# Performance work log

Measured on AMD Instinct MI355X. Metric: run time of the kernel, lower is better.

The kernel has to match this reference:

```python
import jax, jax.numpy as jnp
import numpy as np

BATCH, SEQ, D_MODEL, STATE_DIM = 2, 4096, 1024, 16
LN_EPS = 1e-5
IMP_TEMP = 0.5


def setup_inputs() -> dict:
    key = jax.random.key(0)
    ks = jax.random.split(key, 7)
    std = 0.02
    x = jax.random.normal(ks[0], (BATCH, SEQ, D_MODEL), jnp.float32)
    A_log = jax.random.normal(ks[1], (D_MODEL, STATE_DIM), jnp.float32) * 0.1
    # Linear weights stored as [in, out] so y = x @ W (same math as torch x @ W.T)
    W_delta = jax.random.normal(ks[2], (D_MODEL, D_MODEL), jnp.float32) * std
    W_B = jax.random.normal(ks[3], (D_MODEL, STATE_DIM), jnp.float32) * std
    W_C = jax.random.normal(ks[4], (D_MODEL, STATE_DIM), jnp.float32) * std
    W_ctx = jax.random.normal(ks[5], (D_MODEL, D_MODEL), jnp.float32) * std
    W_imp = jax.random.normal(ks[6], (D_MODEL, D_MODEL), jnp.float32) * std
    ln_gamma = jnp.ones((D_MODEL,), jnp.float32)
    ln_beta = jnp.zeros((D_MODEL,), jnp.float32)
    context_scale = jnp.asarray(0.1, jnp.float32)
    return dict(x=x, A_log=A_log, W_delta=W_delta, W_B=W_B, W_C=W_C,
                ln_gamma=ln_gamma, ln_beta=ln_beta, W_ctx=W_ctx,
                context_scale=context_scale, W_imp=W_imp)


def _selective_scan(x, delta, A, B_sel, C_sel):
    # x, delta: [B,S,D]; A: [D,N]; B_sel, C_sel: [B,S,N]
    Bsz, S, D = x.shape
    N = A.shape[1]
    h0 = jnp.zeros((Bsz, D, N), x.dtype)

    def step(h, inp):
        d_t, x_t, b_t, c_t = inp  # [B,D],[B,D],[B,N],[B,N]
        decay = jnp.exp(d_t[:, :, None] * A)             # [B,D,N]
        h = h * decay + (d_t * x_t)[:, :, None] * b_t[:, None, :]
        y = jnp.einsum('bdn,bn->bd', h, c_t)
        return h, y

    xs = (delta.transpose(1, 0, 2), x.transpose(1, 0, 2),
          B_sel.transpose(1, 0, 2), C_sel.transpose(1, 0, 2))
    _, ys = jax.lax.scan(step, h0, xs)                    # ys: [S,B,D]
    return ys.transpose(1, 0, 2)


def _layernorm(x, gamma, beta):
    mu = jnp.mean(x, axis=-1, keepdims=True)
    var = jnp.mean((x - mu) ** 2, axis=-1, keepdims=True)
    return (x - mu) * jax.lax.rsqrt(var + LN_EPS) * gamma + beta


def reference(x, A_log, W_delta, W_B, W_C, ln_gamma, ln_beta, W_ctx, context_scale, W_imp):
    delta = jax.nn.softplus(x @ W_delta)          # [B,S,D]
    B_sel = x @ W_B                               # [B,S,N]
    C_sel = x @ W_C                               # [B,S,N]
    A = -jnp.exp(A_log)                           # [D,N]
    ssm_out = _selective_scan(x, delta, A, B_sel, C_sel)
    ssm_out = _layernorm(ssm_out, ln_gamma, ln_beta)
    h_final = ssm_out[:, -1, :]                   # [B,D]
    h_proj = h_final @ W_imp                      # [B,D]
    raw_importance = jnp.einsum('bsd,bd->bs', x, h_proj)
    importance = jax.nn.softmax(raw_importance / IMP_TEMP, axis=-1)
    context = (ssm_out @ W_ctx) * context_scale
    return importance, context, raw_importance
```

## Files before the change

kernel.cpp:

```cpp
#include <hip/hip_runtime.h>
#include <hip/hip_bf16.h>
#include <stdint.h>

#define DEV static __device__ __forceinline__

typedef unsigned short u16;
typedef __bf16 bf16x8 __attribute__((ext_vector_type(8)));
typedef float f32x4 __attribute__((ext_vector_type(4)));
typedef u16 u16x8 __attribute__((ext_vector_type(8)));
typedef u16 u16x4 __attribute__((ext_vector_type(4)));

#define IMP_OFF 0
#define CTX_OFF 8192
#define RAW_OFF 8396800

DEV float b2f(u16 u) {
    union { unsigned int i; float f; } v; v.i = ((unsigned int)u) << 16; return v.f;
}
DEV u16 f2b(float f) {
    union { float f; unsigned int i; } v; v.f = f;
    unsigned int r = v.i + 0x7fffu + ((v.i >> 16) & 1u);
    return (u16)(r >> 16);
}
DEV u16 f2h(float f) {
    union { _Float16 h; u16 u; } v; v.h = (_Float16)f; return v.u;
}
DEV float h2f(u16 u) {
    union { u16 u; _Float16 h; } v; v.u = u; return (float)v.h;
}
DEV float softplus_f(float z) {
    float a = fabsf(z);
    return fmaxf(z, 0.f) + __logf(1.f + __expf(-a));
}
DEV float ldin(const void* p, size_t i, int f32) {
    return f32 ? ((const float*)p)[i] : b2f(((const u16*)p)[i]);
}
DEV void stout(void* base, size_t i, float v, int f32) {
    if (f32) ((float*)base)[i] = v;
    else     ((u16*)base)[i] = f2b(v);
}

typedef __attribute__((address_space(1))) void as1_void;
typedef __attribute__((address_space(3))) void as3_void;
DEV void gld_lds16(const void* g, void* l) {
    __builtin_amdgcn_global_load_lds((as1_void*)g, (as3_void*)l, 16, 0, 0);
}

__global__ void init_k(const void* gamma, const void* scale, int* flg, float* hproj)
{
    int i = blockIdx.x * 256 + threadIdx.x;
    if (i < 2048) hproj[i] = 0.f;
    if (i == 0) {
        unsigned int g = *(const unsigned int*)gamma;
        flg[0] = (g == 0x3F800000u) ? 1 : 0;
        unsigned int s = *(const unsigned int*)scale;
        flg[1] = (s == 0x3DCCCCCDu) ? 1 : 0;
    }
}

__global__ __launch_bounds__(256) void transpose_k(
    const void* __restrict__ s0, const void* __restrict__ s1,
    u16* __restrict__ d0, u16* __restrict__ d1, const int* __restrict__ flg)
{
    __shared__ u16 tile[32][33];
    int f32 = flg[0];
    int blk = blockIdx.x;
    const void* src = (blk < 1024) ? s0 : s1;
    u16* dst = (blk < 1024) ? d0 : d1;
    int t = blk & 1023;
    int tr = t >> 5, tc = t & 31;
    int lx = threadIdx.x & 31, ly = threadIdx.x >> 5;
    int r0 = tr * 32, c0 = tc * 32;
#pragma unroll
    for (int i = 0; i < 32; i += 8)
        tile[ly + i][lx] = f2b(ldin(src, (size_t)(r0 + ly + i) * 1024 + c0 + lx, f32));
    __syncthreads();
#pragma unroll
    for (int i = 0; i < 32; i += 8)
        dst[(size_t)(c0 + ly + i) * 1024 + r0 + lx] = tile[lx][ly + i];
}

__global__ __launch_bounds__(256) void prep_small_k(
    const void* __restrict__ W_B, const void* __restrict__ W_C,
    u16* __restrict__ WdT, const int* __restrict__ flg)
{
    int f32 = flg[0];
    int r = blockIdx.x;
    u16* dst = WdT + (size_t)(1024 + r) * 1024;
#pragma unroll
    for (int i = 0; i < 4; i++) {
        int d = threadIdx.x + i * 256;
        u16 v;
        if (r < 16)       v = f2b(ldin(W_B, (size_t)d * 16 + r, f32));
        else if (r < 32)  v = f2b(ldin(W_C, (size_t)d * 16 + (r - 16), f32));
        else              v = 0;
        dst[d] = v;
    }
}

#define GK 1024
__global__ __launch_bounds__(256) void gemm_bt(
    const void* __restrict__ Av, const u16* __restrict__ BT,
    u16* __restrict__ deltaOut, float* __restrict__ Bsel, float* __restrict__ Csel,
    void* __restrict__ outB, const void* __restrict__ scale_p,
    const int* __restrict__ flg, int nbn, int mode)
{
    __shared__ u16 lA[128 * 32];
    __shared__ u16 lB[128 * 32];
    int af32 = (mode == 0) ? flg[0] : 0;
    int blk = blockIdx.x;
    int xcd = blk & 7;
    int local = blk >> 3;
    int bm = xcd * 8 + local / nbn;
    int bn = local % nbn;
    int tid = threadIdx.x;
    int wave = tid >> 6, lane = tid & 63;
    int wm = wave >> 1, wn = wave & 1;
    int lm = lane & 15, kq = lane >> 4;

    f32x4 acc[4][4];
#pragma unroll
    for (int i = 0; i < 4; i++)
#pragma unroll
        for (int j = 0; j < 4; j++) acc[i][j] = f32x4{0.f, 0.f, 0.f, 0.f};

    const u16* Bb = BT + (size_t)bn * 128 * GK;
    int r0 = tid >> 2, kp0 = tid & 3;
    int c1 = tid + 256;
    int r1 = c1 >> 2, kp1 = c1 & 3;
    size_t ib = (size_t)bm * 128 * GK;

    if (af32) {
        const float* Af = (const float*)Av;
        for (int k0 = 0; k0 < GK; k0 += 32) {
            size_t i0 = ib + (size_t)r0 * GK + k0 + kp0 * 8;
            size_t i1 = ib + (size_t)r1 * GK + k0 + kp1 * 8;
            u16x8 a0, a1, b0, b1;
            f32x4 p0 = *(const f32x4*)(Af + i0);
            f32x4 p1 = *(const f32x4*)(Af + i0 + 4);
            f32x4 q0 = *(const f32x4*)(Af + i1);
            f32x4 q1 = *(const f32x4*)(Af + i1 + 4);
#pragma unroll
            for (int j = 0; j < 4; j++) {
                a0[j] = f2b(p0[j]); a0[4 + j] = f2b(p1[j]);
                a1[j] = f2b(q0[j]); a1[4 + j] = f2b(q1[j]);
            }
            b0 = *(const u16x8*)(Bb + (size_t)r0 * GK + k0 + kp0 * 8);
            b1 = *(const u16x8*)(Bb + (size_t)r1 * GK + k0 + kp1 * 8);
            __syncthreads();
            *(u16x8*)&lA[tid * 8] = a0;
            *(u16x8*)&lA[c1 * 8]  = a1;
            *(u16x8*)&lB[tid * 8] = b0;
            *(u16x8*)&lB[c1 * 8]  = b1;
            __syncthreads();
            bf16x8 af[4], bfr[4];
#pragma unroll
            for (int t = 0; t < 4; t++)
                af[t] = *(const bf16x8*)&lA[(wm * 64 + t * 16 + lm) * 32 + kq * 8];
#pragma unroll
            for (int t = 0; t < 4; t++)
                bfr[t] = *(const bf16x8*)&lB[(wn * 64 + t * 16 + lm) * 32 + kq * 8];
#pragma unroll
            for (int i = 0; i < 4; i++)
#pragma unroll
                for (int j = 0; j < 4; j++)
                    acc[i][j] = __builtin_amdgcn_mfma_f32_16x16x32_bf16(af[i], bfr[j], acc[i][j], 0, 0, 0);
        }
    } else {
        const u16* Au = (const u16*)Av;
        const u16* ga0 = Au + ib + (size_t)r0 * GK + kp0 * 8;
        const u16* ga1 = Au + ib + (size_t)r1 * GK + kp1 * 8;
        const u16* gb0 = Bb + (size_t)r0 * GK + kp0 * 8;
        const u16* gb1 = Bb + (size_t)r1 * GK + kp1 * 8;
        for (int k0 = 0; k0 < GK; k0 += 32) {
            if (k0) __syncthreads();
            gld_lds16(ga0 + k0, &lA[tid * 8]);
            gld_lds16(ga1 + k0, &lA[c1 * 8]);
            gld_lds16(gb0 + k0, &lB[tid * 8]);
            gld_lds16(gb1 + k0, &lB[c1 * 8]);
            __syncthreads();
            bf16x8 af[4], bfr[4];
#pragma unroll
            for (int t = 0; t < 4; t++)
                af[t] = *(const bf16x8*)&lA[(wm * 64 + t * 16 + lm) * 32 + kq * 8];
#pragma unroll
            for (int t = 0; t < 4; t++)
                bfr[t] = *(const bf16x8*)&lB[(wn * 64 + t * 16 + lm) * 32 + kq * 8];
#pragma unroll
            for (int i = 0; i < 4; i++)
#pragma unroll
                for (int j = 0; j < 4; j++)
                    acc[i][j] = __builtin_amdgcn_mfma_f32_16x16x32_bf16(af[i], bfr[j], acc[i][j], 0, 0, 0);
        }
    }

    float sc = 1.f;
    int of32 = 0;
    if (mode == 1) {
        sc = flg[1] ? *(const float*)scale_p : b2f(*(const u16*)scale_p);
        of32 = flg[0];
    }
#pragma unroll
    for (int i = 0; i < 4; i++) {
#pragma unroll
        for (int j = 0; j < 4; j++) {
            int row = bm * 128 + wm * 64 + i * 16 + kq * 4;
            int colg = bn * 128 + wn * 64 + j * 16 + lm;
#pragma unroll
            for (int r = 0; r < 4; r++) {
                float v = acc[i][j][r];
                if (mode == 0) {
                    if (colg < 1024) {
                        deltaOut[(size_t)(row + r) * 1024 + colg] = f2h(softplus_f(v));
                    } else if (colg < 1040) {
                        Bsel[(size_t)(row + r) * 16 + (colg - 1024)] = v;
                    } else if (colg < 1056) {
                        Csel[(size_t)(row + r) * 16 + (colg - 1040)] = v;
                    }
                } else {
                    stout(outB, CTX_OFF + (size_t)(row + r) * 1024 + colg, v * sc, of32);
                }
            }
        }
    }
}

__global__ __launch_bounds__(256) void scan_pass1(
    const u16* __restrict__ delta, const void* __restrict__ x,
    const void* __restrict__ A_log, const float* __restrict__ Bsel,
    float* __restrict__ P, float* __restrict__ Hend, const int* __restrict__ flg)
{
    int f32 = flg[0];
    int blk = blockIdx.x;
    int dblk = blk & 3;
    int c = (blk >> 2) & 63;
    int b = blk >> 8;
    int d = dblk * 256 + threadIdx.x;

    float A[16];
#pragma unroll
    for (int n = 0; n < 16; n++) A[n] = -__expf(ldin(A_log, (size_t)d * 16 + n, f32));

    float h[16], Pr[16];
#pragma unroll
    for (int n = 0; n < 16; n++) { h[n] = 0.f; Pr[n] = 1.f; }

    int t0 = c * 64;
    size_t rb = ((size_t)b * 4096 + t0) * 1024 + d;
    size_t bb = ((size_t)b * 4096 + t0) * 16;

    for (int t = 0; t < 64; t++) {
        size_t idx = rb + (size_t)t * 1024;
        float dl = h2f(delta[idx]);
        float xv = ldin(x, idx, f32);
        float du = dl * xv;
        f32x4 Bq[4];
#pragma unroll
        for (int q = 0; q < 4; q++) Bq[q] = *(const f32x4*)&Bsel[bb + t * 16 + q * 4];
#pragma unroll
        for (int n = 0; n < 16; n++) {
            float dec = __expf(dl * A[n]);
            Pr[n] *= dec;
            h[n] = h[n] * dec + du * Bq[n >> 2][n & 3];
        }
    }
    size_t o = (((size_t)(b * 64 + c)) * 1024 + d) * 16;
#pragma unroll
    for (int q = 0; q < 4; q++) {
        *(f32x4*)&P[o + q * 4]    = f32x4{Pr[q*4], Pr[q*4+1], Pr[q*4+2], Pr[q*4+3]};
        *(f32x4*)&Hend[o + q * 4] = f32x4{h[q*4], h[q*4+1], h[q*4+2], h[q*4+3]};
    }
}

__global__ __launch_bounds__(256) void scan_pass2(
    float* __restrict__ P, const float* __restrict__ Hend)
{
    int idx = blockIdx.x * 256 + threadIdx.x;
    int n = idx & 15;
    int d = (idx >> 4) & 1023;
    int b = idx >> 14;
    float h = 0.f;
    for (int c = 0; c < 64; c++) {
        size_t o = (((size_t)(b * 64 + c)) * 1024 + d) * 16 + n;
        float p = P[o];
        float he = Hend[o];
        P[o] = h;
        h = h * p + he;
    }
}

__global__ __launch_bounds__(256) void scan_pass3(
    u16* __restrict__ dssm, const void* __restrict__ x,
    const void* __restrict__ A_log, const float* __restrict__ Bsel,
    const float* __restrict__ Csel, const float* __restrict__ Hinit,
    const int* __restrict__ flg)
{
    int f32 = flg[0];
    int blk = blockIdx.x;
    int dblk = blk & 3;
    int c = (blk >> 2) & 63;
    int b = blk >> 8;
    int d = dblk * 256 + threadIdx.x;

    float A[16];
#pragma unroll
    for (int n = 0; n < 16; n++) A[n] = -__expf(ldin(A_log, (size_t)d * 16 + n, f32));

    float h[16];
    size_t o = (((size_t)(b * 64 + c)) * 1024 + d) * 16;
#pragma unroll
    for (int q = 0; q < 4; q++) {
        f32x4 hq = *(const f32x4*)&Hinit[o + q * 4];
#pragma unroll
        for (int e = 0; e < 4; e++) h[q * 4 + e] = hq[e];
    }

    int t0 = c * 64;
    size_t rb = ((size_t)b * 4096 + t0) * 1024 + d;
    size_t bb = ((size_t)b * 4096 + t0) * 16;

    for (int t = 0; t < 64; t++) {
        size_t idx = rb + (size_t)t * 1024;
        float dl = h2f(dssm[idx]);
        float xv = ldin(x, idx, f32);
        float du = dl * xv;
        f32x4 Bq[4], Cq[4];
#pragma unroll
        for (int q = 0; q < 4; q++) Bq[q] = *(const f32x4*)&Bsel[bb + t * 16 + q * 4];
#pragma unroll
        for (int q = 0; q < 4; q++) Cq[q] = *(const f32x4*)&Csel[bb + t * 16 + q * 4];
        float y = 0.f;
#pragma unroll
        for (int n = 0; n < 16; n++) {
            float dec = __expf(dl * A[n]);
            h[n] = h[n] * dec + du * Bq[n >> 2][n & 3];
            y += h[n] * Cq[n >> 2][n & 3];
        }
        dssm[idx] = f2b(y);
    }
}

__global__ __launch_bounds__(256) void ln_kernel(
    u16* __restrict__ dssm, const void* __restrict__ gamma,
    const void* __restrict__ beta, const int* __restrict__ flg)
{
    int f32 = flg[0];
    int row = blockIdx.x;
    int tid = threadIdx.x;
    u16* p = dssm + (size_t)row * 1024;
    u16x4 raw = *(const u16x4*)&p[tid * 4];
    float v0 = b2f(raw[0]), v1 = b2f(raw[1]), v2 = b2f(raw[2]), v3 = b2f(raw[3]);
    float s = v0 + v1 + v2 + v3;
    float sq = v0*v0 + v1*v1 + v2*v2 + v3*v3;
#pragma unroll
    for (int off = 32; off > 0; off >>= 1) {
        s += __shfl_down(s, off);
        sq += __shfl_down(sq, off);
    }
    __shared__ float rs[4], rq[4];
    int wave = tid >> 6, lane = tid & 63;
    if (lane == 0) { rs[wave] = s; rq[wave] = sq; }
    __syncthreads();
    s = rs[0] + rs[1] + rs[2] + rs[3];
    sq = rq[0] + rq[1] + rq[2] + rq[3];
    float mu = s * (1.f / 1024.f);
    float var = sq * (1.f / 1024.f) - mu * mu;
    float rstd = rsqrtf(fmaxf(var, 0.f) + 1e-5f);
    float vv[4] = {v0, v1, v2, v3};
    u16x4 o4;
#pragma unroll
    for (int i = 0; i < 4; i++) {
        float g = ldin(gamma, (size_t)tid * 4 + i, f32);
        float bt = ldin(beta, (size_t)tid * 4 + i, f32);
        o4[i] = f2b((vv[i] - mu) * rstd * g + bt);
    }
    *(u16x4*)&p[tid * 4] = o4;
}

__global__ __launch_bounds__(256) void hproj_kernel(
    const u16* __restrict__ ssm_ln, const void* __restrict__ W_imp,
    float* __restrict__ hproj, const int* __restrict__ flg)
{
    int f32 = flg[0];
    int blk = blockIdx.x;
    int kc = blk >> 2;
    int g = blk & 3;
    int col = g * 256 + threadIdx.x;
    const u16* h0 = ssm_ln + (size_t)4095 * 1024;
    const u16* h1 = ssm_ln + (size_t)8191 * 1024;
    float a0 = 0.f, a1 = 0.f;
#pragma unroll
    for (int r = 0; r < 32; r++) {
        int d = kc * 32 + r;
        float wv = ldin(W_imp, (size_t)d * 1024 + col, f32);
        a0 += b2f(h0[d]) * wv;
        a1 += b2f(h1[d]) * wv;
    }
    atomicAdd(&hproj[col], a0);
    atomicAdd(&hproj[1024 + col], a1);
}

__global__ __launch_bounds__(256) void raw_kernel(
    const void* __restrict__ x, const float* __restrict__ hproj,
    float* __restrict__ rawF, void* __restrict__ outB, const int* __restrict__ flg)
{
    __shared__ float hp[1024];
    int f32 = flg[0];
    int blk = blockIdx.x;
    int row0 = blk * 4;
    int b = row0 >> 12;
    int tid = threadIdx.x;
#pragma unroll
    for (int i = 0; i < 4; i++) hp[tid + i * 256] = hproj[(size_t)b * 1024 + tid + i * 256];
    __syncthreads();
    int wave = tid >> 6, lane = tid & 63;
    int row = row0 + wave;
    float acc = 0.f;
    if (f32) {
        const float* xr = (const float*)x + (size_t)row * 1024;
#pragma unroll
        for (int half = 0; half < 2; half++) {
            f32x4 x0 = *(const f32x4*)&xr[half * 512 + lane * 8];
            f32x4 x1 = *(const f32x4*)&xr[half * 512 + lane * 8 + 4];
            f32x4 h0 = *(const f32x4*)&hp[half * 512 + lane * 8];
            f32x4 h1 = *(const f32x4*)&hp[half * 512 + lane * 8 + 4];
#pragma unroll
            for (int j = 0; j < 4; j++) { acc += x0[j] * h0[j]; acc += x1[j] * h1[j]; }
        }
    } else {
        const u16* xr = (const u16*)x + (size_t)row * 1024;
#pragma unroll
        for (int half = 0; half < 2; half++) {
            u16x8 xv = *(const u16x8*)&xr[half * 512 + lane * 8];
            f32x4 h0 = *(const f32x4*)&hp[half * 512 + lane * 8];
            f32x4 h1 = *(const f32x4*)&hp[half * 512 + lane * 8 + 4];
#pragma unroll
            for (int j = 0; j < 4; j++) {
                acc += b2f(xv[j]) * h0[j];
                acc += b2f(xv[4 + j]) * h1[j];
            }
        }
    }
#pragma unroll
    for (int off = 32; off > 0; off >>= 1) acc += __shfl_down(acc, off);
    if (lane == 0) { rawF[row] = acc; stout(outB, RAW_OFF + row, acc, f32); }
}

__global__ __launch_bounds__(256) void softmax_kernel(
    const float* __restrict__ rawF, void* __restrict__ outB, const int* __restrict__ flg)
{
    int f32 = flg[0];
    int b = blockIdx.x;
    int tid = threadIdx.x;
    int wave = tid >> 6, lane = tid & 63;
    float v[16];
    float mx = -1e30f;
#pragma unroll
    for (int i = 0; i < 16; i++) {
        v[i] = rawF[(size_t)b * 4096 + i * 256 + tid];
        mx = fmaxf(mx, v[i]);
    }
#pragma unroll
    for (int off = 32; off > 0; off >>= 1) mx = fmaxf(mx, __shfl_xor(mx, off));
    __shared__ float redm[4], reds[4];
    if (lane == 0) redm[wave] = mx;
    __syncthreads();
    mx = fmaxf(fmaxf(redm[0], redm[1]), fmaxf(redm[2], redm[3]));
    float s = 0.f;
#pragma unroll
    for (int i = 0; i < 16; i++) {
        v[i] = __expf(2.f * (v[i] - mx));
        s += v[i];
    }
#pragma unroll
    for (int off = 32; off > 0; off >>= 1) s += __shfl_xor(s, off);
    if (lane == 0) reds[wave] = s;
    __syncthreads();
    s = reds[0] + reds[1] + reds[2] + reds[3];
    float inv = 1.f / s;
#pragma unroll
    for (int i = 0; i < 16; i++)
        stout(outB, IMP_OFF + (size_t)b * 4096 + i * 256 + tid, v[i] * inv, f32);
}

extern "C" void kernel_launch(void* const* d_in, const int* in_sizes, int n_in,
                              void* d_out, int out_size, void* d_ws, size_t ws_size,
                              hipStream_t stream)
{
    const void* x       = d_in[0];
    const void* A_log   = d_in[1];
    const void* W_delta = d_in[2];
    const void* W_B     = d_in[3];
    const void* W_C     = d_in[4];
    const void* gamma   = d_in[5];
    const void* beta    = d_in[6];
    const void* W_ctx   = d_in[7];
    const void* scale   = d_in[8];
    const void* W_imp   = d_in[9];

    char* w = (char*)d_ws;
    u16* WdT    = (u16*)w;   w += (size_t)1152 * 1024 * 2;
    u16* WcT    = (u16*)w;   w += (size_t)1024 * 1024 * 2;
    u16* dssm   = (u16*)w;   w += (size_t)8192 * 1024 * 2;
    float* Bsel = (float*)w; w += (size_t)8192 * 16 * 4;
    float* Csel = (float*)w; w += (size_t)8192 * 16 * 4;
    float* P    = (float*)w; w += (size_t)2 * 64 * 1024 * 16 * 4;
    float* Hend = (float*)w; w += (size_t)2 * 64 * 1024 * 16 * 4;
    float* hproj= (float*)w; w += (size_t)2 * 1024 * 4;
    float* rawF = (float*)w; w += (size_t)8192 * 4;
    int* flg    = (int*)w;   w += 16;

    init_k<<<8, 256, 0, stream>>>(gamma, scale, flg, hproj);
    transpose_k<<<2048, 256, 0, stream>>>(W_delta, W_ctx, WdT, WcT, flg);
    prep_small_k<<<128, 256, 0, stream>>>(W_B, W_C, WdT, flg);
    gemm_bt<<<576, 256, 0, stream>>>(x, WdT, dssm, Bsel, Csel, nullptr, nullptr, flg, 9, 0);
    scan_pass1<<<512, 256, 0, stream>>>(dssm, x, A_log, Bsel, P, Hend, flg);
    scan_pass2<<<128, 256, 0, stream>>>(P, Hend);
    scan_pass3<<<512, 256, 0, stream>>>(dssm, x, A_log, Bsel, Csel, P, flg);
    ln_kernel<<<8192, 256, 0, stream>>>(dssm, gamma, beta, flg);
    hproj_kernel<<<128, 256, 0, stream>>>(dssm, W_imp, hproj, flg);
    raw_kernel<<<2048, 256, 0, stream>>>(x, hproj, rawF, d_out, flg);
    softmax_kernel<<<2, 256, 0, stream>>>(rawF, d_out, flg);
    gemm_bt<<<512, 256, 0, stream>>>(dssm, WcT, nullptr, nullptr, nullptr, d_out, scale, flg, 8, 1);
}
```

Measured before the change: 318.7 us.

## Double GEMM K-tile to 64 and XOR-swizzle LDS layout against bank conflicts

The bf16 MFMA GEMM now stages 64-wide K slices instead of 32, so it needs half as many barrier pairs per K loop and issues more MFMAs per synchronization. The global-to-LDS loads permute the 8-element chunk index by XOR with the row, and the fragment reads apply the same swizzle. This is meant to avoid LDS bank conflicts on the strided row reads. LDS use doubles to 32 KB per block, which could lower occupancy.

```diff
diff --git a/kernel.cpp b/kernel.cpp
--- a/kernel.cpp
+++ b/kernel.cpp
@@ -105,8 +105,8 @@
     void* __restrict__ outB, const void* __restrict__ scale_p,
     const int* __restrict__ flg, int nbn, int mode)
 {
-    __shared__ u16 lA[128 * 32];
-    __shared__ u16 lB[128 * 32];
+    __shared__ u16 lA[128 * 64];
+    __shared__ u16 lB[128 * 64];
     int af32 = (mode == 0) ? flg[0] : 0;
     int blk = blockIdx.x;
     int xcd = blk & 7;
@@ -125,72 +125,77 @@
         for (int j = 0; j < 4; j++) acc[i][j] = f32x4{0.f, 0.f, 0.f, 0.f};
 
     const u16* Bb = BT + (size_t)bn * 128 * GK;
-    int r0 = tid >> 2, kp0 = tid & 3;
-    int c1 = tid + 256;
-    int r1 = c1 >> 2, kp1 = c1 & 3;
     size_t ib = (size_t)bm * 128 * GK;
+
+    int rr = tid >> 3;
+    int kpg = (tid & 7) ^ (rr & 7);
+    size_t soff = (size_t)rr * GK + (size_t)kpg * 8;
+    int ldsl = tid * 8;
+    int lmslot = lm & 7;
 
     if (af32) {
         const float* Af = (const float*)Av;
-        for (int k0 = 0; k0 < GK; k0 += 32) {
-            size_t i0 = ib + (size_t)r0 * GK + k0 + kp0 * 8;
-            size_t i1 = ib + (size_t)r1 * GK + k0 + kp1 * 8;
-            u16x8 a0, a1, b0, b1;
-            f32x4 p0 = *(const f32x4*)(Af + i0);
-            f32x4 p1 = *(const f32x4*)(Af + i0 + 4);
-            f32x4 q0 = *(const f32x4*)(Af + i1);
-            f32x4 q1 = *(const f32x4*)(Af + i1 + 4);
-#pragma unroll
-            for (int j = 0; j < 4; j++) {
-                a0[j] = f2b(p0[j]); a0[4 + j] = f2b(p1[j]);
-                a1[j] = f2b(q0[j]); a1[4 + j] = f2b(q1[j]);
-            }
-            b0 = *(const u16x8*)(Bb + (size_t)r0 * GK + k0 + kp0 * 8);
-            b1 = *(const u16x8*)(Bb + (size_t)r1 * GK + k0 + kp1 * 8);
+        for (int k0 = 0; k0 < GK; k0 += 64) {
+            u16x8 a[4], b[4];
+#pragma unroll
+            for (int w = 0; w < 4; w++) {
+                size_t so = ib + soff + (size_t)w * 32 * GK + k0;
+                f32x4 p0 = *(const f32x4*)(Af + so);
+                f32x4 p1 = *(const f32x4*)(Af + so + 4);
+#pragma unroll
+                for (int j = 0; j < 4; j++) { a[w][j] = f2b(p0[j]); a[w][4 + j] = f2b(p1[j]); }
+                b[w] = *(const u16x8*)(Bb + soff + (size_t)w * 32 * GK + k0);
+            }
             __syncthreads();
-            *(u16x8*)&lA[tid * 8] = a0;
-            *(u16x8*)&lA[c1 * 8]  = a1;
-            *(u16x8*)&lB[tid * 8] = b0;
-            *(u16x8*)&lB[c1 * 8]  = b1;
+#pragma unroll
+            for (int w = 0; w < 4; w++) {
+                *(u16x8*)&lA[ldsl + w * 2048] = a[w];
+                *(u16x8*)&lB[ldsl + w * 2048] = b[w];
+            }
             __syncthreads();
-            bf16x8 af[4], bfr[4];
-#pragma unroll
-            for (int t = 0; t < 4; t++)
-                af[t] = *(const bf16x8*)&lA[(wm * 64 + t * 16 + lm) * 32 + kq * 8];
-#pragma unroll
-            for (int t = 0; t < 4; t++)
-                bfr[t] = *(const bf16x8*)&lB[(wn * 64 + t * 16 + lm) * 32 + kq * 8];
-#pragma unroll
-            for (int i = 0; i < 4; i++)
-#pragma unroll
-                for (int j = 0; j < 4; j++)
-                    acc[i][j] = __builtin_amdgcn_mfma_f32_16x16x32_bf16(af[i], bfr[j], acc[i][j], 0, 0, 0);
+#pragma unroll
+            for (int h = 0; h < 2; h++) {
+                int slot = ((h * 4 + kq) ^ lmslot) * 8;
+                bf16x8 af[4], bfr[4];
+#pragma unroll
+                for (int t = 0; t < 4; t++) {
+                    af[t]  = *(const bf16x8*)&lA[(wm * 64 + t * 16 + lm) * 64 + slot];
+                    bfr[t] = *(const bf16x8*)&lB[(wn * 64 + t * 16 + lm) * 64 + slot];
+                }
+#pragma unroll
+                for (int i = 0; i < 4; i++)
+#pragma unroll
+                    for (int j = 0; j < 4; j++)
+                        acc[i][j] = __builtin_amdgcn_mfma_f32_16x16x32_bf16(af[i], bfr[j], acc[i][j], 0, 0, 0);
+            }
         }
     } else {
         const u16* Au = (const u16*)Av;
-        const u16* ga0 = Au + ib + (size_t)r0 * GK + kp0 * 8;
-        const u16* ga1 = Au + ib + (size_t)r1 * GK + kp1 * 8;
-        const u16* gb0 = Bb + (size_t)r0 * GK + kp0 * 8;
-        const u16* gb1 = Bb + (size_t)r1 * GK + kp1 * 8;
-        for (int k0 = 0; k0 < GK; k0 += 32) {
+        const u16* Aw = Au + ib + soff;
+        const u16* Bw = Bb + soff;
+        for (int k0 = 0; k0 < GK; k0 += 64) {
             if (k0) __syncthreads();
-            gld_lds16(ga0 + k0, &lA[tid * 8]);
-            gld_lds16(ga1 + k0, &lA[c1 * 8]);
-            gld_lds16(gb0 + k0, &lB[tid * 8]);
-            gld_lds16(gb1 + k0, &lB[c1 * 8]);
+#pragma unroll
+            for (int w = 0; w < 4; w++) {
+                gld_lds16(Aw + (size_t)w * 32 * GK + k0, &lA[ldsl + w * 2048]);
+                gld_lds16(Bw + (size_t)w * 32 * GK + k0, &lB[ldsl + w * 2048]);
+            }
             __syncthreads();
-            bf16x8 af[4], bfr[4];
-#pragma unroll
-            for (int t = 0; t < 4; t++)
-                af[t] = *(const bf16x8*)&lA[(wm * 64 + t * 16 + lm) * 32 + kq * 8];
-#pragma unroll
-            for (int t = 0; t < 4; t++)
-                bfr[t] = *(const bf16x8*)&lB[(wn * 64 + t * 16 + lm) * 32 + kq * 8];
-#pragma unroll
-            for (int i = 0; i < 4; i++)
-#pragma unroll
-                for (int j = 0; j < 4; j++)
-                    acc[i][j] = __builtin_amdgcn_mfma_f32_16x16x32_bf16(af[i], bfr[j], acc[i][j], 0, 0, 0);
+#pragma unroll
+            for (int h = 0; h < 2; h++) {
+                int slot = ((h * 4 + kq) ^ lmslot) * 8;
+                bf16x8 af[4], bfr[4];
+#pragma unroll
+                for (int t = 0; t < 4; t++) {
+                    af[t]  = *(const bf16x8*)&lA[(wm * 64 + t * 16 + lm) * 64 + slot];
+                    bfr[t] = *(const bf16x8*)&lB[(wn * 64 + t * 16 + lm) * 64 + slot];
+                }
+#pragma unroll
+                for (int i = 0; i < 4; i++)
+#pragma unroll
+                    for (int j = 0; j < 4; j++)
+                        acc[i][j] = __builtin_amdgcn_mfma_f32_16x16x32_bf16(af[i], bfr[j], acc[i][j], 0, 0, 0);
+            }
         }
     }
 
```

Measured after the change: 324.3 us. Within noise of the previous version (+1.7%).

## Shrink GEMM N-tile to 64, swizzle LDS layout, unroll scan pass2

Applied to the files above, without the earlier changes.

Both GEMMs now use 128x64 tiles instead of 128x128, which doubles the grid and lowers accumulator register use. The LDS tile gets an XOR swizzle so MFMA fragment reads avoid bank conflicts. Scan pass2 is unrolled by four so its loads are issued ahead of the serial recurrence. The cost is less A-tile reuse per block, so more global reads of A.

```diff
diff --git a/kernel.cpp b/kernel.cpp
--- a/kernel.cpp
+++ b/kernel.cpp
@@ -106,7 +106,7 @@
     const int* __restrict__ flg, int nbn, int mode)
 {
     __shared__ u16 lA[128 * 32];
-    __shared__ u16 lB[128 * 32];
+    __shared__ u16 lB[64 * 32];
     int af32 = (mode == 0) ? flg[0] : 0;
     int blk = blockIdx.x;
     int xcd = blk & 7;
@@ -118,78 +118,78 @@
     int wm = wave >> 1, wn = wave & 1;
     int lm = lane & 15, kq = lane >> 4;
 
-    f32x4 acc[4][4];
+    f32x4 acc[4][2];
 #pragma unroll
     for (int i = 0; i < 4; i++)
 #pragma unroll
-        for (int j = 0; j < 4; j++) acc[i][j] = f32x4{0.f, 0.f, 0.f, 0.f};
-
-    const u16* Bb = BT + (size_t)bn * 128 * GK;
-    int r0 = tid >> 2, kp0 = tid & 3;
-    int c1 = tid + 256;
-    int r1 = c1 >> 2, kp1 = c1 & 3;
+        for (int j = 0; j < 2; j++) acc[i][j] = f32x4{0.f, 0.f, 0.f, 0.f};
+
+    const u16* Bb = BT + (size_t)bn * 64 * GK;
     size_t ib = (size_t)bm * 128 * GK;
+
+    int rr = tid >> 2;
+    int gg = (tid & 3) ^ ((tid >> 3) & 3);
+    size_t soff = (size_t)rr * GK + (size_t)gg * 8;
+    int slot = (kq ^ ((lm >> 1) & 3)) * 8;
 
     if (af32) {
         const float* Af = (const float*)Av;
         for (int k0 = 0; k0 < GK; k0 += 32) {
-            size_t i0 = ib + (size_t)r0 * GK + k0 + kp0 * 8;
-            size_t i1 = ib + (size_t)r1 * GK + k0 + kp1 * 8;
-            u16x8 a0, a1, b0, b1;
-            f32x4 p0 = *(const f32x4*)(Af + i0);
-            f32x4 p1 = *(const f32x4*)(Af + i0 + 4);
-            f32x4 q0 = *(const f32x4*)(Af + i1);
-            f32x4 q1 = *(const f32x4*)(Af + i1 + 4);
-#pragma unroll
-            for (int j = 0; j < 4; j++) {
-                a0[j] = f2b(p0[j]); a0[4 + j] = f2b(p1[j]);
-                a1[j] = f2b(q0[j]); a1[4 + j] = f2b(q1[j]);
+            u16x8 a0, a1, b0;
+            {
+                size_t s0 = ib + soff + k0;
+                size_t s1 = ib + (size_t)64 * GK + soff + k0;
+                f32x4 p0 = *(const f32x4*)(Af + s0);
+                f32x4 p1 = *(const f32x4*)(Af + s0 + 4);
+                f32x4 q0 = *(const f32x4*)(Af + s1);
+                f32x4 q1 = *(const f32x4*)(Af + s1 + 4);
+#pragma unroll
+                for (int j = 0; j < 4; j++) {
+                    a0[j] = f2b(p0[j]); a0[4 + j] = f2b(p1[j]);
+                    a1[j] = f2b(q0[j]); a1[4 + j] = f2b(q1[j]);
+                }
+                b0 = *(const u16x8*)(Bb + soff + k0);
             }
-            b0 = *(const u16x8*)(Bb + (size_t)r0 * GK + k0 + kp0 * 8);
-            b1 = *(const u16x8*)(Bb + (size_t)r1 * GK + k0 + kp1 * 8);
             __syncthreads();
-            *(u16x8*)&lA[tid * 8] = a0;
-            *(u16x8*)&lA[c1 * 8]  = a1;
-            *(u16x8*)&lB[tid * 8] = b0;
-            *(u16x8*)&lB[c1 * 8]  = b1;
+            *(u16x8*)&lA[tid * 8]        = a0;
+            *(u16x8*)&lA[2048 + tid * 8] = a1;
+            *(u16x8*)&lB[tid * 8]        = b0;
             __syncthreads();
-            bf16x8 af[4], bfr[4];
+            bf16x8 af[4], bfr[2];
 #pragma unroll
             for (int t = 0; t < 4; t++)
-                af[t] = *(const bf16x8*)&lA[(wm * 64 + t * 16 + lm) * 32 + kq * 8];
-#pragma unroll
-            for (int t = 0; t < 4; t++)
-                bfr[t] = *(const bf16x8*)&lB[(wn * 64 + t * 16 + lm) * 32 + kq * 8];
+                af[t] = *(const bf16x8*)&lA[(wm * 64 + t * 16 + lm) * 32 + slot];
+#pragma unroll
+            for (int j = 0; j < 2; j++)
+                bfr[j] = *(const bf16x8*)&lB[(wn * 32 + j * 16 + lm) * 32 + slot];
 #pragma unroll
             for (int i = 0; i < 4; i++)
 #pragma unroll
-                for (int j = 0; j < 4; j++)
+                for (int j = 0; j < 2; j++)
                     acc[i][j] = __builtin_amdgcn_mfma_f32_16x16x32_bf16(af[i], bfr[j], acc[i][j], 0, 0, 0);
         }
     } else {
         const u16* Au = (const u16*)Av;
-        const u16* ga0 = Au + ib + (size_t)r0 * GK + kp0 * 8;
-        const u16* ga1 = Au + ib + (size_t)r1 * GK + kp1 * 8;
-        const u16* gb0 = Bb + (size_t)r0 * GK + kp0 * 8;
-        const u16* gb1 = Bb + (size_t)r1 * GK + kp1 * 8;
+        const u16* A0 = Au + ib + soff;
+        const u16* A1 = Au + ib + (size_t)64 * GK + soff;
+        const u16* B0 = Bb + soff;
         for (int k0 = 0; k0 < GK; k0 += 32) {
             if (k0) __syncthreads();
-            gld_lds16(ga0 + k0, &lA[tid * 8]);
-            gld_lds16(ga1 + k0, &lA[c1 * 8]);
-            gld_lds16(gb0 + k0, &lB[tid * 8]);
-            gld_lds16(gb1 + k0, &lB[c1 * 8]);
+            gld_lds16(A0 + k0, &lA[tid * 8]);
+            gld_lds16(A1 + k0, &lA[2048 + tid * 8]);
+            gld_lds16(B0 + k0, &lB[tid * 8]);
             __syncthreads();
-            bf16x8 af[4], bfr[4];
+            bf16x8 af[4], bfr[2];
 #pragma unroll
             for (int t = 0; t < 4; t++)
-                af[t] = *(const bf16x8*)&lA[(wm * 64 + t * 16 + lm) * 32 + kq * 8];
-#pragma unroll
-            for (int t = 0; t < 4; t++)
-                bfr[t] = *(const bf16x8*)&lB[(wn * 64 + t * 16 + lm) * 32 + kq * 8];
+                af[t] = *(const bf16x8*)&lA[(wm * 64 + t * 16 + lm) * 32 + slot];
+#pragma unroll
+            for (int j = 0; j < 2; j++)
+                bfr[j] = *(const bf16x8*)&lB[(wn * 32 + j * 16 + lm) * 32 + slot];
 #pragma unroll
             for (int i = 0; i < 4; i++)
 #pragma unroll
-                for (int j = 0; j < 4; j++)
+                for (int j = 0; j < 2; j++)
                     acc[i][j] = __builtin_amdgcn_mfma_f32_16x16x32_bf16(af[i], bfr[j], acc[i][j], 0, 0, 0);
         }
     }
@@ -203,9 +203,9 @@
 #pragma unroll
     for (int i = 0; i < 4; i++) {
 #pragma unroll
-        for (int j = 0; j < 4; j++) {
+        for (int j = 0; j < 2; j++) {
             int row = bm * 128 + wm * 64 + i * 16 + kq * 4;
-            int colg = bn * 128 + wn * 64 + j * 16 + lm;
+            int colg = bn * 64 + wn * 32 + j * 16 + lm;
 #pragma unroll
             for (int r = 0; r < 4; r++) {
                 float v = acc[i][j][r];
@@ -279,13 +279,20 @@
     int n = idx & 15;
     int d = (idx >> 4) & 1023;
     int b = idx >> 14;
+    size_t base = (((size_t)(b * 64)) * 1024 + d) * 16 + n;
+    const size_t step = (size_t)1024 * 16;
     float h = 0.f;
-    for (int c = 0; c < 64; c++) {
-        size_t o = (((size_t)(b * 64 + c)) * 1024 + d) * 16 + n;
-        float p = P[o];
-        float he = Hend[o];
-        P[o] = h;
-        h = h * p + he;
+    for (int c = 0; c < 64; c += 4) {
+        size_t o0 = base + (size_t)c * step;
+        size_t o1 = o0 + step, o2 = o0 + 2 * step, o3 = o0 + 3 * step;
+        float p0 = P[o0], e0 = Hend[o0];
+        float p1 = P[o1], e1 = Hend[o1];
+        float p2 = P[o2], e2 = Hend[o2];
+        float p3 = P[o3], e3 = Hend[o3];
+        P[o0] = h; h = h * p0 + e0;
+        P[o1] = h; h = h * p1 + e1;
+        P[o2] = h; h = h * p2 + e2;
+        P[o3] = h; h = h * p3 + e3;
     }
 }
 
@@ -513,7 +520,7 @@
     init_k<<<8, 256, 0, stream>>>(gamma, scale, flg, hproj);
     transpose_k<<<2048, 256, 0, stream>>>(W_delta, W_ctx, WdT, WcT, flg);
     prep_small_k<<<128, 256, 0, stream>>>(W_B, W_C, WdT, flg);
-    gemm_bt<<<576, 256, 0, stream>>>(x, WdT, dssm, Bsel, Csel, nullptr, nullptr, flg, 9, 0);
+    gemm_bt<<<1088, 256, 0, stream>>>(x, WdT, dssm, Bsel, Csel, nullptr, nullptr, flg, 17, 0);
     scan_pass1<<<512, 256, 0, stream>>>(dssm, x, A_log, Bsel, P, Hend, flg);
     scan_pass2<<<128, 256, 0, stream>>>(P, Hend);
     scan_pass3<<<512, 256, 0, stream>>>(dssm, x, A_log, Bsel, Csel, P, flg);
@@ -521,5 +528,5 @@
     hproj_kernel<<<128, 256, 0, stream>>>(dssm, W_imp, hproj, flg);
     raw_kernel<<<2048, 256, 0, stream>>>(x, hproj, rawF, d_out, flg);
     softmax_kernel<<<2, 256, 0, stream>>>(rawF, d_out, flg);
-    gemm_bt<<<512, 256, 0, stream>>>(dssm, WcT, nullptr, nullptr, nullptr, d_out, scale, flg, 8, 1);
-}
+    gemm_bt<<<1024, 256, 0, stream>>>(dssm, WcT, nullptr, nullptr, nullptr, d_out, scale, flg, 16, 1);
+}
```

Measured after the change: 318.5 us. No clear change (-0.1%).
